# Optimization experiments

Hardware: AMD Instinct MI355X
Metric: run time of the kernel (lower is better)

Reference implementation:

```python
import jax, jax.numpy as jnp
import numpy as np

B, T, F, H, V = 16, 512, 512, 2048, 64
INPUT_INT_SCALE = 3.0
INT16_MIN, INT16_MAX = -32768, 32767


def setup_inputs() -> dict:
    key = jax.random.key(0)
    ks = jax.random.split(key, 8)
    x = jax.random.normal(ks[0], (B, T, F), dtype=jnp.float32)
    # int4 weights stored as int32 in [-8, 7]
    W_res_i4 = jax.random.randint(ks[1], (H, H), -8, 8, dtype=jnp.int32)
    W_in_i4 = jax.random.randint(ks[2], (H, F), -8, 8, dtype=jnp.int32)
    # per-row quantization scales (positive)
    S_res_row = jax.random.uniform(ks[3], (H,), dtype=jnp.float32, minval=0.01, maxval=0.2)
    S_in_row = jax.random.uniform(ks[4], (H,), dtype=jnp.float32, minval=0.01, maxval=0.2)
    g_res = jnp.float32(1.0)
    g_in = jnp.float32(1.0)
    W_out_w = jax.random.normal(ks[5], (V, H), dtype=jnp.float32) / np.float32(np.sqrt(H))
    W_out_b = jnp.zeros((V,), dtype=jnp.float32)
    return {
        "x": x, "S_res_row": S_res_row, "S_in_row": S_in_row,
        "g_res": g_res, "g_in": g_in,
        "W_out_w": W_out_w, "W_out_b": W_out_b,
        "W_res_i4": W_res_i4, "W_in_i4": W_in_i4,
    }


def reference(x, S_res_row, S_in_row, g_res, g_in, W_out_w, W_out_b, W_res_i4, W_in_i4):
    # row scales (matches _row_scales)
    s_res = (S_res_row / 49.0 * g_res)[None, :]                     # (1,H)
    s_in = (S_in_row / (7.0 * max(1.0, INPUT_INT_SCALE)) * g_in)[None, :]  # (1,H)

    def step(h, x_t):
        # quantize input frame and hidden state to integers (detached in torch)
        u_int = jax.lax.stop_gradient(jnp.round(x_t * INPUT_INT_SCALE)).astype(jnp.int32)     # (B,F)
        h_int = jax.lax.stop_gradient(jnp.round(jnp.clip(h, -1.0, 1.0) * 7.0)).astype(jnp.int32)  # (B,H)
        # integer matvecs: y[b,k] = sum_j W[k,j] * v[b,j]
        out_res = jnp.einsum('bh,kh->bk', h_int, W_res_i4)  # (B,H) int32
        out_in = jnp.einsum('bf,kf->bk', u_int, W_in_i4)    # (B,H) int32
        # int16 saturation, then row scale + gain, tanh
        out_res_f = jnp.clip(out_res, INT16_MIN, INT16_MAX).astype(jnp.float32)
        out_in_f = jnp.clip(out_in, INT16_MIN, INT16_MAX).astype(jnp.float32)
        h_new = jnp.tanh(out_res_f * s_res + out_in_f * s_in)
        return h_new, h_new

    h0 = jnp.zeros((x.shape[0], W_res_i4.shape[0]), dtype=jnp.float32)
    _, Hs = jax.lax.scan(step, h0, jnp.swapaxes(x, 0, 1))  # (T,B,H)
    Hs = jnp.swapaxes(Hs, 0, 1)                            # (B,T,H)
    # readout
    return jnp.einsum('bth,vh->btv', Hs, W_out_w) + W_out_b
```

## Files before the change

kernel.cpp:

```cpp
#include <hip/hip_runtime.h>
#include <hip/hip_bf16.h>


#define B_ 16
#define T_ 512
#define F_ 512
#define H_ 2048
#define V_ 64
#define SLICES 32
#define RPW 64
#define NTHREADS 256
#define NWG 512

typedef int i4v __attribute__((ext_vector_type(4)));

#if defined(__has_builtin)
#if __has_builtin(__builtin_amdgcn_sdot8)
#define HAVE_SDOT8 1
#endif
#endif

__device__ __forceinline__ int sdot8(int a, int b, int c) {
#ifdef HAVE_SDOT8
  return __builtin_amdgcn_sdot8(a, b, c, false);
#else
#pragma unroll
  for (int i = 0; i < 8; ++i) {
    int av = (a << (28 - 4 * i)) >> 28;
    int bv = (b << (28 - 4 * i)) >> 28;
    c += av * bv;
  }
  return c;
#endif
}

__device__ __forceinline__ float tanh_ref(float x) {
  float ax = fabsf(x);
  float xc = fminf(fmaxf(x, -7.90531110763549805f), 7.90531110763549805f);
  float x2 = __fmul_rn(xc, xc);
  float p = -2.76076847742355e-16f;
  p = __fmaf_rn(x2, p, 2.00018790482477e-13f);
  p = __fmaf_rn(x2, p, -8.60467152213735e-11f);
  p = __fmaf_rn(x2, p, 5.12229709037114e-08f);
  p = __fmaf_rn(x2, p, 1.48572235717979e-05f);
  p = __fmaf_rn(x2, p, 6.37261928875436e-04f);
  p = __fmaf_rn(x2, p, 4.89352455891786e-03f);
  p = __fmul_rn(xc, p);
  float q = 1.19825839466702e-06f;
  q = __fmaf_rn(x2, q, 1.18534705686654e-04f);
  q = __fmaf_rn(x2, q, 2.26843463243900e-03f);
  q = __fmaf_rn(x2, q, 4.89352518554385e-03f);
  float r = __fdiv_rn(p, q);
  return (ax < 0.0004f) ? x : r;
}

__device__ __forceinline__ unsigned f2bf(float f) {
  unsigned u = __float_as_uint(f);
  return (u + 0x7fffu + ((u >> 16) & 1u)) >> 16;
}

__device__ __forceinline__ void publish_tag(unsigned long long* p, unsigned data, unsigned tag) {
  unsigned long long u = ((unsigned long long)tag << 32) | data;
  __hip_atomic_store(p, u, __ATOMIC_RELAXED, __HIP_MEMORY_SCOPE_AGENT);
}

__global__ void pack_weights(const int* __restrict__ Wres, const int* __restrict__ Win,
                             int* __restrict__ wr4, int* __restrict__ wi4) {
  int id = blockIdx.x * blockDim.x + threadIdx.x;
  if (id < H_ * 256) {
    const int* src = Wres + id * 8;
    int pk = 0;
#pragma unroll
    for (int i = 0; i < 8; ++i) pk |= (src[i] & 15) << (4 * i);
    wr4[id] = pk;
  } else {
    int id2 = id - H_ * 256;
    if (id2 < H_ * 64) {
      const int* src = Win + id2 * 8;
      int pk = 0;
#pragma unroll
      for (int i = 0; i < 8; ++i) pk |= (src[i] & 15) << (4 * i);
      wi4[id2] = pk;
    }
  }
}

__global__ void pack_u(const float* __restrict__ x, int* __restrict__ um, int* __restrict__ ua) {
  int idx = blockIdx.x * blockDim.x + threadIdx.x;
  if (idx >= B_ * T_ * 64) return;
  const float* src = x + (size_t)idx * 8;
  int pm = 0, pa = 0;
#pragma unroll
  for (int i = 0; i < 8; ++i) {
    int u = (int)rintf(__fmul_rn(src[i], 3.0f));
    int vv = u + 128;
    pm |= (vv & 7) << (4 * i);
    pa |= (((vv >> 3) - 16) & 15) << (4 * i);
  }
  um[idx] = pm;
  ua[idx] = pa;
}

#define WLD(i, OFFSTR) \
  asm volatile("ds_read_b128 %0, %1 offset:" OFFSTR : "=v"(wreg[i]) : "v"(lds_wb))

__global__ void __launch_bounds__(NTHREADS, 2) esn_main(
    const int* __restrict__ um, const int* __restrict__ ua,
    const int* __restrict__ wr4, const int* __restrict__ wi4,
    unsigned long long* hq2,
    const float* __restrict__ S_res, const float* __restrict__ S_in,
    const float* __restrict__ g_res, const float* __restrict__ g_in,
    unsigned* __restrict__ Hs, int t0, int t1) {
  extern __shared__ __align__(16) char smem[];
  ::int4* lw4 = (::int4*)smem;
  int* lds_h = (int*)(lw4 + 16 * 256);
  int* lds_u = lds_h + 2 * 272;

  const int wg = blockIdx.x;
  const int b = wg & 15, slice = wg >> 4;
  const int tid = threadIdx.x;
  const unsigned lane = tid & 63;
  const int q = tid & 3;
  const int grow = slice * RPW + (tid >> 2);

  {
    const ::int4* gw = (const ::int4*)wr4;
#pragma unroll 4
    for (int m = 0; m < 16; ++m) lw4[m * 256 + tid] = gw[grow * 64 + q * 16 + m];
  }
  ::int4 rwm[4];
  {
    const ::int4* gwi = (const ::int4*)wi4;
#pragma unroll
    for (int m = 0; m < 4; ++m) rwm[m] = gwi[grow * 16 + q * 4 + m];
  }
  const float sr = __fmul_rn(__fdiv_rn(S_res[grow], 49.0f), g_res[0]);
  const float si = __fmul_rn(__fdiv_rn(S_in[grow], 21.0f), g_in[0]);

  const unsigned lds_wb = (unsigned)(size_t)smem + (unsigned)tid * 16u;

  unsigned ureg = 0;
  if (tid < 128) {
    unsigned v0 = (tid < 64) ? (unsigned)um[(b * T_ + t0) * 64 + tid]
                             : (unsigned)ua[(b * T_ + t0) * 64 + (tid - 64)];
    lds_u[(t0 & 1) * 128 + tid] = (int)v0;
    if (t0 + 1 < T_)
      ureg = (tid < 64) ? (unsigned)um[(b * T_ + t0 + 1) * 64 + tid]
                        : (unsigned)ua[(b * T_ + t0 + 1) * 64 + (tid - 64)];
  }
  __syncthreads();

  for (int t = t0; t < t1; ++t) {
    const int cbuf = t & 1, nbuf = cbuf ^ 1;
    if (t + 1 < t1 && tid < 128) lds_u[nbuf * 128 + tid] = (int)ureg;

    int am = 0, aa = 0;
    {
      const ::int4* lu = (const ::int4*)(lds_u + cbuf * 128);
#pragma unroll
      for (int m = 0; m < 4; ++m) {
        ::int4 w = rwm[m];
        ::int4 uM = lu[q * 4 + m];
        ::int4 uA = lu[16 + q * 4 + m];
        am = sdot8(w.x, uM.x, am); am = sdot8(w.y, uM.y, am);
        am = sdot8(w.z, uM.z, am); am = sdot8(w.w, uM.w, am);
        aa = sdot8(w.x, uA.x, aa); aa = sdot8(w.y, uA.y, aa);
        aa = sdot8(w.z, uA.z, aa); aa = sdot8(w.w, uA.w, aa);
      }
    }
    int accin = am + (aa << 3);
    accin += __shfl_xor(accin, 1);
    accin += __shfl_xor(accin, 2);

    i4v wreg[16];
    WLD(0, "0");      WLD(1, "4096");   WLD(2, "8192");   WLD(3, "12288");
    WLD(4, "16384");  WLD(5, "20480");  WLD(6, "24576");  WLD(7, "28672");
    WLD(8, "32768");  WLD(9, "36864");  WLD(10, "40960"); WLD(11, "45056");
    WLD(12, "49152"); WLD(13, "53248"); WLD(14, "57344"); WLD(15, "61440");

    if (tid < 64) {
      const unsigned long long* p = hq2 + (size_t)(cbuf * 16 + b) * 256 + tid * 4;
      unsigned long long u0, u1, u2, u3;
      const unsigned tag = (unsigned)t;
      for (;;) {
        u0 = __hip_atomic_load(p + 0, __ATOMIC_RELAXED, __HIP_MEMORY_SCOPE_AGENT);
        u1 = __hip_atomic_load(p + 1, __ATOMIC_RELAXED, __HIP_MEMORY_SCOPE_AGENT);
        u2 = __hip_atomic_load(p + 2, __ATOMIC_RELAXED, __HIP_MEMORY_SCOPE_AGENT);
        u3 = __hip_atomic_load(p + 3, __ATOMIC_RELAXED, __HIP_MEMORY_SCOPE_AGENT);
        unsigned d = ((unsigned)(u0 >> 32) ^ tag) | ((unsigned)(u1 >> 32) ^ tag) |
                     ((unsigned)(u2 >> 32) ^ tag) | ((unsigned)(u3 >> 32) ^ tag);
        if (d == 0) break;
        __builtin_amdgcn_s_sleep(1);
      }
      ::int4 hv;
      hv.x = (int)u0; hv.y = (int)u1; hv.z = (int)u2; hv.w = (int)u3;
      ((::int4*)(lds_h + cbuf * 272))[(tid >> 4) * 17 + (tid & 15)] = hv;
    }

    __syncthreads();
    __builtin_amdgcn_sched_barrier(0);

    int c0 = 0, c1 = 0, c2 = 0, c3 = 0;
    {
      const ::int4* lh = (const ::int4*)(lds_h + cbuf * 272);
#pragma unroll
      for (int m = 0; m < 16; m += 4) {
        ::int4 h0 = lh[q * 17 + m + 0];
        ::int4 h1 = lh[q * 17 + m + 1];
        ::int4 h2 = lh[q * 17 + m + 2];
        ::int4 h3 = lh[q * 17 + m + 3];
        c0 = sdot8(wreg[m + 0].x, h0.x, c0); c0 = sdot8(wreg[m + 0].y, h0.y, c0);
        c0 = sdot8(wreg[m + 0].z, h0.z, c0); c0 = sdot8(wreg[m + 0].w, h0.w, c0);
        c1 = sdot8(wreg[m + 1].x, h1.x, c1); c1 = sdot8(wreg[m + 1].y, h1.y, c1);
        c1 = sdot8(wreg[m + 1].z, h1.z, c1); c1 = sdot8(wreg[m + 1].w, h1.w, c1);
        c2 = sdot8(wreg[m + 2].x, h2.x, c2); c2 = sdot8(wreg[m + 2].y, h2.y, c2);
        c2 = sdot8(wreg[m + 2].z, h2.z, c2); c2 = sdot8(wreg[m + 2].w, h2.w, c2);
        c3 = sdot8(wreg[m + 3].x, h3.x, c3); c3 = sdot8(wreg[m + 3].y, h3.y, c3);
        c3 = sdot8(wreg[m + 3].z, h3.z, c3); c3 = sdot8(wreg[m + 3].w, h3.w, c3);
      }
    }
    int acc = (c0 + c1) + (c2 + c3);
    acc += __shfl_xor(acc, 1);
    acc += __shfl_xor(acc, 2);

    int cr = min(max(acc, -32768), 32767);
    int ci = min(max(accin, -32768), 32767);
    float arg = __fadd_rn(__fmul_rn((float)cr, sr), __fmul_rn((float)ci, si));
    float hn = tanh_ref(arg);
    float hc = fminf(fmaxf(hn, -1.0f), 1.0f);
    int qv = (int)rintf(__fmul_rn(hc, 7.0f));

    unsigned nib = ((unsigned)qv & 15u) << (4 * ((lane >> 2) & 7));
    nib |= (unsigned)__shfl_xor((int)nib, 4);
    nib |= (unsigned)__shfl_xor((int)nib, 8);
    nib |= (unsigned)__shfl_xor((int)nib, 16);
    if ((lane & 31) == 0)
      publish_tag(hq2 + (size_t)((t ^ 1) & 1) * 0 +
                      (size_t)(nbuf * 16 + b) * 256 + slice * 8 + (tid >> 6) * 2 + (lane >> 5),
                  nib, (unsigned)(t + 1));

    unsigned bfb = f2bf(hn);
    unsigned other = (unsigned)__shfl_xor((int)bfb, 4);
    if ((tid & 7) == 0)
      Hs[(size_t)(b * T_ + t) * (H_ / 2) + slice * 32 + (tid >> 3)] = bfb | (other << 16);
    if (t + 2 < T_ && tid < 128)
      ureg = (tid < 64) ? (unsigned)um[(b * T_ + t + 2) * 64 + tid]
                        : (unsigned)ua[(b * T_ + t + 2) * 64 + (tid - 64)];
  }
}

#define ACC8(acc, p, w0, w1)                                    \
  acc = fmaf(__uint_as_float(p.x << 16), w0.x, acc);            \
  acc = fmaf(__uint_as_float(p.x & 0xffff0000u), w0.y, acc);    \
  acc = fmaf(__uint_as_float(p.y << 16), w0.z, acc);            \
  acc = fmaf(__uint_as_float(p.y & 0xffff0000u), w0.w, acc);    \
  acc = fmaf(__uint_as_float(p.z << 16), w1.x, acc);            \
  acc = fmaf(__uint_as_float(p.z & 0xffff0000u), w1.y, acc);    \
  acc = fmaf(__uint_as_float(p.w << 16), w1.z, acc);            \
  acc = fmaf(__uint_as_float(p.w & 0xffff0000u), w1.w, acc);

__global__ void __launch_bounds__(256) readout(const unsigned* __restrict__ Hs,
                                               const float* __restrict__ Wout,
                                               const float* __restrict__ Wb,
                                               float* __restrict__ out) {
  const int v = threadIdx.x & 63;
  const int rg = threadIdx.x >> 6;
  const int bt0 = blockIdx.x * 16 + rg * 4;
  const float* wrow = Wout + (size_t)v * H_;
  const unsigned* h0 = Hs + (size_t)bt0 * (H_ / 2);
  float a0 = Wb[v], a1 = a0, a2 = a0, a3 = a0;
  for (int j = 0; j < H_ / 2; j += 4) {
    float4 w0 = *(const float4*)(wrow + 2 * j);
    float4 w1 = *(const float4*)(wrow + 2 * j + 4);
    uint4 p0 = *(const uint4*)(h0 + j);
    uint4 p1 = *(const uint4*)(h0 + (H_ / 2) + j);
    uint4 p2 = *(const uint4*)(h0 + 2 * (H_ / 2) + j);
    uint4 p3 = *(const uint4*)(h0 + 3 * (H_ / 2) + j);
    ACC8(a0, p0, w0, w1)
    ACC8(a1, p1, w0, w1)
    ACC8(a2, p2, w0, w1)
    ACC8(a3, p3, w0, w1)
  }
  out[(size_t)(bt0 + 0) * V_ + v] = a0;
  out[(size_t)(bt0 + 1) * V_ + v] = a1;
  out[(size_t)(bt0 + 2) * V_ + v] = a2;
  out[(size_t)(bt0 + 3) * V_ + v] = a3;
}

extern "C" void kernel_launch(void* const* d_in, const int* in_sizes, int n_in,
                              void* d_out, int out_size, void* d_ws, size_t ws_size,
                              hipStream_t stream) {
  const float* x = (const float*)d_in[0];
  const float* S_res = (const float*)d_in[1];
  const float* S_in = (const float*)d_in[2];
  const float* g_res = (const float*)d_in[3];
  const float* g_in = (const float*)d_in[4];
  const float* Woutw = (const float*)d_in[5];
  const float* Woutb = (const float*)d_in[6];
  const int* Wres = (const int*)d_in[7];
  const int* Win = (const int*)d_in[8];

  char* ws = (char*)d_ws;
  unsigned long long* hq2 = (unsigned long long*)(ws + 4096);
  int* um = (int*)(ws + (1 << 20));
  int* ua = um + (1 << 19);
  int* wr4 = ua + (1 << 19);
  int* wi4 = wr4 + (1 << 19);
  unsigned* Hs = (unsigned*)(ws + (8 << 20));

  hipMemsetAsync(d_ws, 0, 4096 + 65536, stream);
  hipLaunchKernelGGL(pack_weights, dim3(2560), dim3(256), 0, stream, Wres, Win, wr4, wi4);
  hipLaunchKernelGGL(pack_u, dim3(2048), dim3(256), 0, stream, x, um, ua);

  const int smem_bytes = 65536 + 2 * 272 * 4 + 2 * 128 * 4;
  (void)hipFuncSetAttribute((const void*)esn_main, hipFuncAttributeMaxDynamicSharedMemorySize,
                            smem_bytes);

  int t0 = 0, t1 = T_;
  void* args[] = {&um, &ua, &wr4, &wi4, &hq2, &S_res, &S_in,
                  &g_res, &g_in, &Hs, &t0, &t1};
  hipError_t e = hipLaunchCooperativeKernel((const void*)esn_main, dim3(NWG), dim3(NTHREADS),
                                            args, smem_bytes, stream);
  if (e != hipSuccess) {
    for (int t = 0; t < T_; ++t) {
      hipLaunchKernelGGL(esn_main, dim3(NWG), dim3(NTHREADS), smem_bytes, stream,
                         um, ua, wr4, wi4, hq2, S_res, S_in, g_res, g_in, Hs, t, t + 1);
    }
  }
  hipLaunchKernelGGL(readout, dim3(B_ * T_ / 16), dim3(256), 0, stream,
                     Hs, Woutw, Woutb, (float*)d_out);
}
```

Before: 1.040 ms.

## Make each wave poll hidden state independently and drop block barrier per step

Each of the four waves now spins on the global hidden-state tags itself and writes a private LDS copy, so the per-step __syncthreads is replaced by a wave-local lgkmcnt wait. Input-frame vectors are prefetched straight into registers from global memory instead of being staged through double-buffered LDS. The spin loop also stops sleeping on the first couple of failed polls. This aims to cut block-wide barrier latency on the serial recurrence critical path, at the cost of four times more atomic polling traffic and extra LDS space.

```diff
diff --git a/kernel.cpp b/kernel.cpp
--- a/kernel.cpp
+++ b/kernel.cpp
@@ -114,14 +114,15 @@
   extern __shared__ __align__(16) char smem[];
   ::int4* lw4 = (::int4*)smem;
   int* lds_h = (int*)(lw4 + 16 * 256);
-  int* lds_u = lds_h + 2 * 272;
 
   const int wg = blockIdx.x;
   const int b = wg & 15, slice = wg >> 4;
   const int tid = threadIdx.x;
-  const unsigned lane = tid & 63;
-  const int q = tid & 3;
-  const int grow = slice * RPW + (tid >> 2);
+  const int wv = tid >> 6;
+  const int lane = tid & 63;
+  const int rl = lane >> 2;
+  const int q = lane & 3;
+  const int grow = slice * RPW + wv * 16 + rl;
 
   {
     const ::int4* gw = (const ::int4*)wr4;
@@ -138,39 +139,20 @@
   const float si = __fmul_rn(__fdiv_rn(S_in[grow], 21.0f), g_in[0]);
 
   const unsigned lds_wb = (unsigned)(size_t)smem + (unsigned)tid * 16u;
-
-  unsigned ureg = 0;
-  if (tid < 128) {
-    unsigned v0 = (tid < 64) ? (unsigned)um[(b * T_ + t0) * 64 + tid]
-                             : (unsigned)ua[(b * T_ + t0) * 64 + (tid - 64)];
-    lds_u[(t0 & 1) * 128 + tid] = (int)v0;
-    if (t0 + 1 < T_)
-      ureg = (tid < 64) ? (unsigned)um[(b * T_ + t0 + 1) * 64 + tid]
-                        : (unsigned)ua[(b * T_ + t0 + 1) * 64 + (tid - 64)];
-  }
-  __syncthreads();
+  int* hb = lds_h + wv * 544;
+
+  const ::int4* gum = (const ::int4*)um;
+  const ::int4* gua = (const ::int4*)ua;
+
+  ::int4 uMr[4], uAr[4];
+  {
+    int base = (b * T_ + t0) * 16 + q * 4;
+#pragma unroll
+    for (int m = 0; m < 4; ++m) { uMr[m] = gum[base + m]; uAr[m] = gua[base + m]; }
+  }
 
   for (int t = t0; t < t1; ++t) {
     const int cbuf = t & 1, nbuf = cbuf ^ 1;
-    if (t + 1 < t1 && tid < 128) lds_u[nbuf * 128 + tid] = (int)ureg;
-
-    int am = 0, aa = 0;
-    {
-      const ::int4* lu = (const ::int4*)(lds_u + cbuf * 128);
-#pragma unroll
-      for (int m = 0; m < 4; ++m) {
-        ::int4 w = rwm[m];
-        ::int4 uM = lu[q * 4 + m];
-        ::int4 uA = lu[16 + q * 4 + m];
-        am = sdot8(w.x, uM.x, am); am = sdot8(w.y, uM.y, am);
-        am = sdot8(w.z, uM.z, am); am = sdot8(w.w, uM.w, am);
-        aa = sdot8(w.x, uA.x, aa); aa = sdot8(w.y, uA.y, aa);
-        aa = sdot8(w.z, uA.z, aa); aa = sdot8(w.w, uA.w, aa);
-      }
-    }
-    int accin = am + (aa << 3);
-    accin += __shfl_xor(accin, 1);
-    accin += __shfl_xor(accin, 2);
 
     i4v wreg[16];
     WLD(0, "0");      WLD(1, "4096");   WLD(2, "8192");   WLD(3, "12288");
@@ -178,31 +160,48 @@
     WLD(8, "32768");  WLD(9, "36864");  WLD(10, "40960"); WLD(11, "45056");
     WLD(12, "49152"); WLD(13, "53248"); WLD(14, "57344"); WLD(15, "61440");
 
-    if (tid < 64) {
-      const unsigned long long* p = hq2 + (size_t)(cbuf * 16 + b) * 256 + tid * 4;
-      unsigned long long u0, u1, u2, u3;
+    int am = 0, aa = 0;
+#pragma unroll
+    for (int m = 0; m < 4; ++m) {
+      ::int4 w = rwm[m];
+      ::int4 uM = uMr[m];
+      ::int4 uA = uAr[m];
+      am = sdot8(w.x, uM.x, am); am = sdot8(w.y, uM.y, am);
+      am = sdot8(w.z, uM.z, am); am = sdot8(w.w, uM.w, am);
+      aa = sdot8(w.x, uA.x, aa); aa = sdot8(w.y, uA.y, aa);
+      aa = sdot8(w.z, uA.z, aa); aa = sdot8(w.w, uA.w, aa);
+    }
+    int accin = am + (aa << 3);
+    accin += __shfl_xor(accin, 1);
+    accin += __shfl_xor(accin, 2);
+
+    unsigned long long u0, u1, u2, u3;
+    {
+      const unsigned long long* pp = hq2 + (size_t)(cbuf * 16 + b) * 256 + lane * 4;
       const unsigned tag = (unsigned)t;
+      int fails = 0;
       for (;;) {
-        u0 = __hip_atomic_load(p + 0, __ATOMIC_RELAXED, __HIP_MEMORY_SCOPE_AGENT);
-        u1 = __hip_atomic_load(p + 1, __ATOMIC_RELAXED, __HIP_MEMORY_SCOPE_AGENT);
-        u2 = __hip_atomic_load(p + 2, __ATOMIC_RELAXED, __HIP_MEMORY_SCOPE_AGENT);
-        u3 = __hip_atomic_load(p + 3, __ATOMIC_RELAXED, __HIP_MEMORY_SCOPE_AGENT);
+        u0 = __hip_atomic_load(pp + 0, __ATOMIC_RELAXED, __HIP_MEMORY_SCOPE_AGENT);
+        u1 = __hip_atomic_load(pp + 1, __ATOMIC_RELAXED, __HIP_MEMORY_SCOPE_AGENT);
+        u2 = __hip_atomic_load(pp + 2, __ATOMIC_RELAXED, __HIP_MEMORY_SCOPE_AGENT);
+        u3 = __hip_atomic_load(pp + 3, __ATOMIC_RELAXED, __HIP_MEMORY_SCOPE_AGENT);
         unsigned d = ((unsigned)(u0 >> 32) ^ tag) | ((unsigned)(u1 >> 32) ^ tag) |
                      ((unsigned)(u2 >> 32) ^ tag) | ((unsigned)(u3 >> 32) ^ tag);
         if (d == 0) break;
-        __builtin_amdgcn_s_sleep(1);
+        if (++fails > 2) __builtin_amdgcn_s_sleep(1);
       }
+    }
+    {
       ::int4 hv;
       hv.x = (int)u0; hv.y = (int)u1; hv.z = (int)u2; hv.w = (int)u3;
-      ((::int4*)(lds_h + cbuf * 272))[(tid >> 4) * 17 + (tid & 15)] = hv;
-    }
-
-    __syncthreads();
+      ((::int4*)(hb + cbuf * 272))[(lane >> 4) * 17 + (lane & 15)] = hv;
+    }
+    asm volatile("s_waitcnt lgkmcnt(0)" ::: "memory");
     __builtin_amdgcn_sched_barrier(0);
 
     int c0 = 0, c1 = 0, c2 = 0, c3 = 0;
     {
-      const ::int4* lh = (const ::int4*)(lds_h + cbuf * 272);
+      const ::int4* lh = (const ::int4*)(hb + cbuf * 272);
 #pragma unroll
       for (int m = 0; m < 16; m += 4) {
         ::int4 h0 = lh[q * 17 + m + 0];
@@ -230,22 +229,24 @@
     float hc = fminf(fmaxf(hn, -1.0f), 1.0f);
     int qv = (int)rintf(__fmul_rn(hc, 7.0f));
 
-    unsigned nib = ((unsigned)qv & 15u) << (4 * ((lane >> 2) & 7));
+    unsigned nib = ((unsigned)qv & 15u) << (4 * (rl & 7));
     nib |= (unsigned)__shfl_xor((int)nib, 4);
     nib |= (unsigned)__shfl_xor((int)nib, 8);
     nib |= (unsigned)__shfl_xor((int)nib, 16);
     if ((lane & 31) == 0)
-      publish_tag(hq2 + (size_t)((t ^ 1) & 1) * 0 +
-                      (size_t)(nbuf * 16 + b) * 256 + slice * 8 + (tid >> 6) * 2 + (lane >> 5),
+      publish_tag(hq2 + (size_t)(nbuf * 16 + b) * 256 + slice * 8 + wv * 2 + (lane >> 5),
                   nib, (unsigned)(t + 1));
 
     unsigned bfb = f2bf(hn);
     unsigned other = (unsigned)__shfl_xor((int)bfb, 4);
-    if ((tid & 7) == 0)
-      Hs[(size_t)(b * T_ + t) * (H_ / 2) + slice * 32 + (tid >> 3)] = bfb | (other << 16);
-    if (t + 2 < T_ && tid < 128)
-      ureg = (tid < 64) ? (unsigned)um[(b * T_ + t + 2) * 64 + tid]
-                        : (unsigned)ua[(b * T_ + t + 2) * 64 + (tid - 64)];
+    if ((lane & 7) == 0)
+      Hs[(size_t)(b * T_ + t) * (H_ / 2) + slice * 32 + wv * 8 + (lane >> 3)] =
+          bfb | (other << 16);
+    if (t + 1 < T_) {
+      int base = (b * T_ + t + 1) * 16 + q * 4;
+#pragma unroll
+      for (int m = 0; m < 4; ++m) { uMr[m] = gum[base + m]; uAr[m] = gua[base + m]; }
+    }
   }
 }
 
@@ -312,7 +313,7 @@
   hipLaunchKernelGGL(pack_weights, dim3(2560), dim3(256), 0, stream, Wres, Win, wr4, wi4);
   hipLaunchKernelGGL(pack_u, dim3(2048), dim3(256), 0, stream, x, um, ua);
 
-  const int smem_bytes = 65536 + 2 * 272 * 4 + 2 * 128 * 4;
+  const int smem_bytes = 65536 + 4 * 2 * 272 * 4;
   (void)hipFuncSetAttribute((const void*)esn_main, hipFuncAttributeMaxDynamicSharedMemorySize,
                             smem_bytes);
 
```

Result: slower. 2.537 ms (+143.8%).

## Replace block barrier with per-wave LDS flags and spread hidden-state polling across waves

Applied to the files above, without the earlier changes.

Every thread now polls one 64-bit tagged hidden-state word, instead of wave 0 polling four words per lane. Each wave writes its quarter of the hidden vector to LDS and raises a workgroup-scope release flag, and consumers acquire-spin per quarter before their dot products. This replaces the full __syncthreads and lets the weight LDS loads and the input dot product overlap the global poll. The LDS weight layout is permuted to match the new quarter-wise consumption, which adds spin loops on LDS flags and relies on subtle memory-ordering correctness.

```diff
diff --git a/kernel.cpp b/kernel.cpp
--- a/kernel.cpp
+++ b/kernel.cpp
@@ -13,6 +13,7 @@
 #define NWG 512
 
 typedef int i4v __attribute__((ext_vector_type(4)));
+typedef unsigned long long ull;
 
 #if defined(__has_builtin)
 #if __has_builtin(__builtin_amdgcn_sdot8)
@@ -59,8 +60,11 @@
   return (u + 0x7fffu + ((u >> 16) & 1u)) >> 16;
 }
 
-__device__ __forceinline__ void publish_tag(unsigned long long* p, unsigned data, unsigned tag) {
-  unsigned long long u = ((unsigned long long)tag << 32) | data;
+__device__ __forceinline__ ull xld(const ull* p) {
+  return __hip_atomic_load(p, __ATOMIC_RELAXED, __HIP_MEMORY_SCOPE_AGENT);
+}
+__device__ __forceinline__ void publish_tag(ull* p, unsigned data, unsigned tag) {
+  ull u = ((ull)tag << 32) | data;
   __hip_atomic_store(p, u, __ATOMIC_RELAXED, __HIP_MEMORY_SCOPE_AGENT);
 }
 
@@ -104,10 +108,26 @@
 #define WLD(i, OFFSTR) \
   asm volatile("ds_read_b128 %0, %1 offset:" OFFSTR : "=v"(wreg[i]) : "v"(lds_wb))
 
+#define QDOT(QQ)                                                                     \
+  {                                                                                  \
+    while (__hip_atomic_load(&lds_flag[cbuf * 4 + QQ], __ATOMIC_ACQUIRE,             \
+                             __HIP_MEMORY_SCOPE_WORKGROUP) < t) {}                   \
+    const ::int4* h4 = (const ::int4*)hbase + QQ * 17 + q * 4;                       \
+    ::int4 h0 = h4[0], h1 = h4[1], h2 = h4[2], h3 = h4[3];                           \
+    c0 = sdot8(wreg[QQ * 4 + 0].x, h0.x, c0); c0 = sdot8(wreg[QQ * 4 + 0].y, h0.y, c0); \
+    c0 = sdot8(wreg[QQ * 4 + 0].z, h0.z, c0); c0 = sdot8(wreg[QQ * 4 + 0].w, h0.w, c0); \
+    c1 = sdot8(wreg[QQ * 4 + 1].x, h1.x, c1); c1 = sdot8(wreg[QQ * 4 + 1].y, h1.y, c1); \
+    c1 = sdot8(wreg[QQ * 4 + 1].z, h1.z, c1); c1 = sdot8(wreg[QQ * 4 + 1].w, h1.w, c1); \
+    c2 = sdot8(wreg[QQ * 4 + 2].x, h2.x, c2); c2 = sdot8(wreg[QQ * 4 + 2].y, h2.y, c2); \
+    c2 = sdot8(wreg[QQ * 4 + 2].z, h2.z, c2); c2 = sdot8(wreg[QQ * 4 + 2].w, h2.w, c2); \
+    c3 = sdot8(wreg[QQ * 4 + 3].x, h3.x, c3); c3 = sdot8(wreg[QQ * 4 + 3].y, h3.y, c3); \
+    c3 = sdot8(wreg[QQ * 4 + 3].z, h3.z, c3); c3 = sdot8(wreg[QQ * 4 + 3].w, h3.w, c3); \
+  }
+
 __global__ void __launch_bounds__(NTHREADS, 2) esn_main(
     const int* __restrict__ um, const int* __restrict__ ua,
     const int* __restrict__ wr4, const int* __restrict__ wi4,
-    unsigned long long* hq2,
+    ull* hq,
     const float* __restrict__ S_res, const float* __restrict__ S_in,
     const float* __restrict__ g_res, const float* __restrict__ g_in,
     unsigned* __restrict__ Hs, int t0, int t1) {
@@ -115,18 +135,21 @@
   ::int4* lw4 = (::int4*)smem;
   int* lds_h = (int*)(lw4 + 16 * 256);
   int* lds_u = lds_h + 2 * 272;
+  int* lds_flag = lds_u + 2 * 128;
 
   const int wg = blockIdx.x;
   const int b = wg & 15, slice = wg >> 4;
   const int tid = threadIdx.x;
-  const unsigned lane = tid & 63;
+  const int wv = tid >> 6;
+  const int lane = tid & 63;
   const int q = tid & 3;
   const int grow = slice * RPW + (tid >> 2);
 
   {
     const ::int4* gw = (const ::int4*)wr4;
 #pragma unroll 4
-    for (int m = 0; m < 16; ++m) lw4[m * 256 + tid] = gw[grow * 64 + q * 16 + m];
+    for (int j = 0; j < 16; ++j)
+      lw4[j * 256 + tid] = gw[grow * 64 + (j >> 2) * 16 + q * 4 + (j & 3)];
   }
   ::int4 rwm[4];
   {
@@ -139,6 +162,7 @@
 
   const unsigned lds_wb = (unsigned)(size_t)smem + (unsigned)tid * 16u;
 
+  if (tid < 8) lds_flag[tid] = -1;
   unsigned ureg = 0;
   if (tid < 128) {
     unsigned v0 = (tid < 64) ? (unsigned)um[(b * T_ + t0) * 64 + tid]
@@ -153,6 +177,15 @@
   for (int t = t0; t < t1; ++t) {
     const int cbuf = t & 1, nbuf = cbuf ^ 1;
     if (t + 1 < t1 && tid < 128) lds_u[nbuf * 128 + tid] = (int)ureg;
+
+    const ull* pp = hq + (size_t)(cbuf * 16 + b) * 256 + tid;
+    ull uv = xld(pp);
+
+    i4v wreg[16];
+    WLD(0, "0");      WLD(1, "4096");   WLD(2, "8192");   WLD(3, "12288");
+    WLD(4, "16384");  WLD(5, "20480");  WLD(6, "24576");  WLD(7, "28672");
+    WLD(8, "32768");  WLD(9, "36864");  WLD(10, "40960"); WLD(11, "45056");
+    WLD(12, "49152"); WLD(13, "53248"); WLD(14, "57344"); WLD(15, "61440");
 
     int am = 0, aa = 0;
     {
@@ -172,53 +205,24 @@
     accin += __shfl_xor(accin, 1);
     accin += __shfl_xor(accin, 2);
 
-    i4v wreg[16];
-    WLD(0, "0");      WLD(1, "4096");   WLD(2, "8192");   WLD(3, "12288");
-    WLD(4, "16384");  WLD(5, "20480");  WLD(6, "24576");  WLD(7, "28672");
-    WLD(8, "32768");  WLD(9, "36864");  WLD(10, "40960"); WLD(11, "45056");
-    WLD(12, "49152"); WLD(13, "53248"); WLD(14, "57344"); WLD(15, "61440");
-
-    if (tid < 64) {
-      const unsigned long long* p = hq2 + (size_t)(cbuf * 16 + b) * 256 + tid * 4;
-      unsigned long long u0, u1, u2, u3;
-      const unsigned tag = (unsigned)t;
-      for (;;) {
-        u0 = __hip_atomic_load(p + 0, __ATOMIC_RELAXED, __HIP_MEMORY_SCOPE_AGENT);
-        u1 = __hip_atomic_load(p + 1, __ATOMIC_RELAXED, __HIP_MEMORY_SCOPE_AGENT);
-        u2 = __hip_atomic_load(p + 2, __ATOMIC_RELAXED, __HIP_MEMORY_SCOPE_AGENT);
-        u3 = __hip_atomic_load(p + 3, __ATOMIC_RELAXED, __HIP_MEMORY_SCOPE_AGENT);
-        unsigned d = ((unsigned)(u0 >> 32) ^ tag) | ((unsigned)(u1 >> 32) ^ tag) |
-                     ((unsigned)(u2 >> 32) ^ tag) | ((unsigned)(u3 >> 32) ^ tag);
-        if (d == 0) break;
-        __builtin_amdgcn_s_sleep(1);
-      }
-      ::int4 hv;
-      hv.x = (int)u0; hv.y = (int)u1; hv.z = (int)u2; hv.w = (int)u3;
-      ((::int4*)(lds_h + cbuf * 272))[(tid >> 4) * 17 + (tid & 15)] = hv;
-    }
-
-    __syncthreads();
-    __builtin_amdgcn_sched_barrier(0);
-
-    int c0 = 0, c1 = 0, c2 = 0, c3 = 0;
     {
-      const ::int4* lh = (const ::int4*)(lds_h + cbuf * 272);
-#pragma unroll
-      for (int m = 0; m < 16; m += 4) {
-        ::int4 h0 = lh[q * 17 + m + 0];
-        ::int4 h1 = lh[q * 17 + m + 1];
-        ::int4 h2 = lh[q * 17 + m + 2];
-        ::int4 h3 = lh[q * 17 + m + 3];
-        c0 = sdot8(wreg[m + 0].x, h0.x, c0); c0 = sdot8(wreg[m + 0].y, h0.y, c0);
-        c0 = sdot8(wreg[m + 0].z, h0.z, c0); c0 = sdot8(wreg[m + 0].w, h0.w, c0);
-        c1 = sdot8(wreg[m + 1].x, h1.x, c1); c1 = sdot8(wreg[m + 1].y, h1.y, c1);
-        c1 = sdot8(wreg[m + 1].z, h1.z, c1); c1 = sdot8(wreg[m + 1].w, h1.w, c1);
-        c2 = sdot8(wreg[m + 2].x, h2.x, c2); c2 = sdot8(wreg[m + 2].y, h2.y, c2);
-        c2 = sdot8(wreg[m + 2].z, h2.z, c2); c2 = sdot8(wreg[m + 2].w, h2.w, c2);
-        c3 = sdot8(wreg[m + 3].x, h3.x, c3); c3 = sdot8(wreg[m + 3].y, h3.y, c3);
-        c3 = sdot8(wreg[m + 3].z, h3.z, c3); c3 = sdot8(wreg[m + 3].w, h3.w, c3);
+      const unsigned tg = (unsigned)t;
+      int fails = 0;
+      while ((unsigned)(uv >> 32) != tg) {
+        if (++fails > 1) __builtin_amdgcn_s_sleep(1);
+        uv = xld(pp);
       }
     }
+    lds_h[cbuf * 272 + wv * 68 + lane] = (int)uv;
+    if (lane == 0)
+      __hip_atomic_store(&lds_flag[cbuf * 4 + wv], t, __ATOMIC_RELEASE,
+                         __HIP_MEMORY_SCOPE_WORKGROUP);
+    asm volatile("s_waitcnt lgkmcnt(0)" ::: "memory");
+    __builtin_amdgcn_sched_barrier(0);
+
+    int c0 = 0, c1 = 0, c2 = 0, c3 = 0;
+    const int* hbase = lds_h + cbuf * 272;
+    QDOT(0) QDOT(1) QDOT(2) QDOT(3)
     int acc = (c0 + c1) + (c2 + c3);
     acc += __shfl_xor(acc, 1);
     acc += __shfl_xor(acc, 2);
@@ -235,8 +239,7 @@
     nib |= (unsigned)__shfl_xor((int)nib, 8);
     nib |= (unsigned)__shfl_xor((int)nib, 16);
     if ((lane & 31) == 0)
-      publish_tag(hq2 + (size_t)((t ^ 1) & 1) * 0 +
-                      (size_t)(nbuf * 16 + b) * 256 + slice * 8 + (tid >> 6) * 2 + (lane >> 5),
+      publish_tag(hq + (size_t)(nbuf * 16 + b) * 256 + slice * 8 + wv * 2 + (lane >> 5),
                   nib, (unsigned)(t + 1));
 
     unsigned bfb = f2bf(hn);
@@ -301,30 +304,30 @@
   const int* Win = (const int*)d_in[8];
 
   char* ws = (char*)d_ws;
-  unsigned long long* hq2 = (unsigned long long*)(ws + 4096);
+  ull* hq = (ull*)(ws + 4096);
   int* um = (int*)(ws + (1 << 20));
   int* ua = um + (1 << 19);
   int* wr4 = ua + (1 << 19);
   int* wi4 = wr4 + (1 << 19);
   unsigned* Hs = (unsigned*)(ws + (8 << 20));
 
-  hipMemsetAsync(d_ws, 0, 4096 + 65536, stream);
+  hipMemsetAsync(ws + 4096, 0, 65536, stream);
   hipLaunchKernelGGL(pack_weights, dim3(2560), dim3(256), 0, stream, Wres, Win, wr4, wi4);
   hipLaunchKernelGGL(pack_u, dim3(2048), dim3(256), 0, stream, x, um, ua);
 
-  const int smem_bytes = 65536 + 2 * 272 * 4 + 2 * 128 * 4;
+  const int smem_bytes = 65536 + 2 * 272 * 4 + 2 * 128 * 4 + 8 * 4;
   (void)hipFuncSetAttribute((const void*)esn_main, hipFuncAttributeMaxDynamicSharedMemorySize,
                             smem_bytes);
 
   int t0 = 0, t1 = T_;
-  void* args[] = {&um, &ua, &wr4, &wi4, &hq2, &S_res, &S_in,
+  void* args[] = {&um, &ua, &wr4, &wi4, &hq, &S_res, &S_in,
                   &g_res, &g_in, &Hs, &t0, &t1};
   hipError_t e = hipLaunchCooperativeKernel((const void*)esn_main, dim3(NWG), dim3(NTHREADS),
                                             args, smem_bytes, stream);
   if (e != hipSuccess) {
     for (int t = 0; t < T_; ++t) {
       hipLaunchKernelGGL(esn_main, dim3(NWG), dim3(NTHREADS), smem_bytes, stream,
-                         um, ua, wr4, wi4, hq2, S_res, S_in, g_res, g_in, Hs, t, t + 1);
+                         um, ua, wr4, wi4, hq, S_res, S_in, g_res, g_in, Hs, t, t + 1);
     }
   }
   hipLaunchKernelGGL(readout, dim3(B_ * T_ / 16), dim3(256), 0, stream,
```

New measurement: 1.946 ms. 1.87x slower.

## Quantize hidden state via precomputed tanh thresholds and double-issue flag polling

Applied to the files above, without the earlier changes.

A setup kernel binary-searches seven input thresholds at which the quantized tanh output steps. The recurrent kernel then produces the int4 hidden value with comparisons instead of a rational tanh, so the next step's value is published before the tanh needed for the bf16 output is computed. The spin-wait now keeps two batches of atomic loads in flight and drops the per-iteration sleep, which shortens the inter-workgroup sync latency on the critical path at the cost of more memory traffic while waiting. Correctness relies on the quantized tanh being monotone in its argument, so that thresholds reproduce rounding exactly.

```diff
diff --git a/kernel.cpp b/kernel.cpp
--- a/kernel.cpp
+++ b/kernel.cpp
@@ -13,6 +13,7 @@
 #define NWG 512
 
 typedef int i4v __attribute__((ext_vector_type(4)));
+typedef unsigned long long ull;
 
 #if defined(__has_builtin)
 #if __has_builtin(__builtin_amdgcn_sdot8)
@@ -54,14 +55,35 @@
   return (ax < 0.0004f) ? x : r;
 }
 
+__device__ __forceinline__ int qv_of(float arg) {
+  float hn = tanh_ref(arg);
+  float hc = fminf(fmaxf(hn, -1.0f), 1.0f);
+  return (int)rintf(__fmul_rn(hc, 7.0f));
+}
+
 __device__ __forceinline__ unsigned f2bf(float f) {
   unsigned u = __float_as_uint(f);
   return (u + 0x7fffu + ((u >> 16) & 1u)) >> 16;
 }
 
-__device__ __forceinline__ void publish_tag(unsigned long long* p, unsigned data, unsigned tag) {
-  unsigned long long u = ((unsigned long long)tag << 32) | data;
+__device__ __forceinline__ ull xld(const ull* p) {
+  return __hip_atomic_load(p, __ATOMIC_RELAXED, __HIP_MEMORY_SCOPE_AGENT);
+}
+__device__ __forceinline__ void publish_tag(ull* p, unsigned data, unsigned tag) {
+  ull u = ((ull)tag << 32) | data;
   __hip_atomic_store(p, u, __ATOMIC_RELAXED, __HIP_MEMORY_SCOPE_AGENT);
+}
+
+__global__ void find_th(float* __restrict__ th) {
+  if (blockIdx.x == 0 && threadIdx.x < 7) {
+    int k = threadIdx.x + 1;
+    unsigned lo = 0, hi = 0x41000000u;
+    while (hi - lo > 1) {
+      unsigned mid = lo + ((hi - lo) >> 1);
+      if (qv_of(__uint_as_float(mid)) >= k) hi = mid; else lo = mid;
+    }
+    th[k - 1] = __uint_as_float(hi);
+  }
 }
 
 __global__ void pack_weights(const int* __restrict__ Wres, const int* __restrict__ Win,
@@ -104,12 +126,19 @@
 #define WLD(i, OFFSTR) \
   asm volatile("ds_read_b128 %0, %1 offset:" OFFSTR : "=v"(wreg[i]) : "v"(lds_wb))
 
+#define TAGOK(V) \
+  (!((((unsigned)(V##0 >> 32)) ^ tg) | (((unsigned)(V##1 >> 32)) ^ tg) | \
+     (((unsigned)(V##2 >> 32)) ^ tg) | (((unsigned)(V##3 >> 32)) ^ tg)))
+#define ISSUE(V) \
+  V##0 = xld(pp); V##1 = xld(pp + 1); V##2 = xld(pp + 2); V##3 = xld(pp + 3);
+
 __global__ void __launch_bounds__(NTHREADS, 2) esn_main(
     const int* __restrict__ um, const int* __restrict__ ua,
     const int* __restrict__ wr4, const int* __restrict__ wi4,
-    unsigned long long* hq2,
+    ull* hq,
     const float* __restrict__ S_res, const float* __restrict__ S_in,
     const float* __restrict__ g_res, const float* __restrict__ g_in,
+    const float* __restrict__ th,
     unsigned* __restrict__ Hs, int t0, int t1) {
   extern __shared__ __align__(16) char smem[];
   ::int4* lw4 = (::int4*)smem;
@@ -136,6 +165,8 @@
   }
   const float sr = __fmul_rn(__fdiv_rn(S_res[grow], 49.0f), g_res[0]);
   const float si = __fmul_rn(__fdiv_rn(S_in[grow], 21.0f), g_in[0]);
+  const float th1 = th[0], th2 = th[1], th3 = th[2], th4 = th[3],
+              th5 = th[4], th6 = th[5], th7 = th[6];
 
   const unsigned lds_wb = (unsigned)(size_t)smem + (unsigned)tid * 16u;
 
@@ -179,21 +210,21 @@
     WLD(12, "49152"); WLD(13, "53248"); WLD(14, "57344"); WLD(15, "61440");
 
     if (tid < 64) {
-      const unsigned long long* p = hq2 + (size_t)(cbuf * 16 + b) * 256 + tid * 4;
-      unsigned long long u0, u1, u2, u3;
-      const unsigned tag = (unsigned)t;
+      const ull* pp = hq + (size_t)(cbuf * 16 + b) * 256 + tid * 4;
+      const unsigned tg = (unsigned)t;
+      ull A0, A1, A2, A3, B0, B1, B2, B3, r0, r1, r2, r3;
+      ISSUE(A)
+      ISSUE(B)
+      int guard = 0;
       for (;;) {
-        u0 = __hip_atomic_load(p + 0, __ATOMIC_RELAXED, __HIP_MEMORY_SCOPE_AGENT);
-        u1 = __hip_atomic_load(p + 1, __ATOMIC_RELAXED, __HIP_MEMORY_SCOPE_AGENT);
-        u2 = __hip_atomic_load(p + 2, __ATOMIC_RELAXED, __HIP_MEMORY_SCOPE_AGENT);
-        u3 = __hip_atomic_load(p + 3, __ATOMIC_RELAXED, __HIP_MEMORY_SCOPE_AGENT);
-        unsigned d = ((unsigned)(u0 >> 32) ^ tag) | ((unsigned)(u1 >> 32) ^ tag) |
-                     ((unsigned)(u2 >> 32) ^ tag) | ((unsigned)(u3 >> 32) ^ tag);
-        if (d == 0) break;
-        __builtin_amdgcn_s_sleep(1);
+        if (TAGOK(A)) { r0 = A0; r1 = A1; r2 = A2; r3 = A3; break; }
+        ISSUE(A)
+        if (TAGOK(B)) { r0 = B0; r1 = B1; r2 = B2; r3 = B3; break; }
+        ISSUE(B)
+        if (++guard > 4096) __builtin_amdgcn_s_sleep(1);
       }
       ::int4 hv;
-      hv.x = (int)u0; hv.y = (int)u1; hv.z = (int)u2; hv.w = (int)u3;
+      hv.x = (int)r0; hv.y = (int)r1; hv.z = (int)r2; hv.w = (int)r3;
       ((::int4*)(lds_h + cbuf * 272))[(tid >> 4) * 17 + (tid & 15)] = hv;
     }
 
@@ -226,19 +257,21 @@
     int cr = min(max(acc, -32768), 32767);
     int ci = min(max(accin, -32768), 32767);
     float arg = __fadd_rn(__fmul_rn((float)cr, sr), __fmul_rn((float)ci, si));
-    float hn = tanh_ref(arg);
-    float hc = fminf(fmaxf(hn, -1.0f), 1.0f);
-    int qv = (int)rintf(__fmul_rn(hc, 7.0f));
+    float av = fabsf(arg);
+    int qa = (av >= th1) + (av >= th2) + (av >= th3) + (av >= th4) +
+             (av >= th5) + (av >= th6) + (av >= th7);
+    int qv = (arg < 0.0f) ? -qa : qa;
 
     unsigned nib = ((unsigned)qv & 15u) << (4 * ((lane >> 2) & 7));
     nib |= (unsigned)__shfl_xor((int)nib, 4);
     nib |= (unsigned)__shfl_xor((int)nib, 8);
     nib |= (unsigned)__shfl_xor((int)nib, 16);
     if ((lane & 31) == 0)
-      publish_tag(hq2 + (size_t)((t ^ 1) & 1) * 0 +
-                      (size_t)(nbuf * 16 + b) * 256 + slice * 8 + (tid >> 6) * 2 + (lane >> 5),
+      publish_tag(hq + (size_t)(nbuf * 16 + b) * 256 + slice * 8 + (tid >> 6) * 2 +
+                      (lane >> 5),
                   nib, (unsigned)(t + 1));
 
+    float hn = tanh_ref(arg);
     unsigned bfb = f2bf(hn);
     unsigned other = (unsigned)__shfl_xor((int)bfb, 4);
     if ((tid & 7) == 0)
@@ -301,14 +334,16 @@
   const int* Win = (const int*)d_in[8];
 
   char* ws = (char*)d_ws;
-  unsigned long long* hq2 = (unsigned long long*)(ws + 4096);
+  float* th = (float*)(ws + 2048);
+  ull* hq = (ull*)(ws + 4096);
   int* um = (int*)(ws + (1 << 20));
   int* ua = um + (1 << 19);
   int* wr4 = ua + (1 << 19);
   int* wi4 = wr4 + (1 << 19);
   unsigned* Hs = (unsigned*)(ws + (8 << 20));
 
-  hipMemsetAsync(d_ws, 0, 4096 + 65536, stream);
+  hipMemsetAsync(ws + 4096, 0, 65536, stream);
+  hipLaunchKernelGGL(find_th, dim3(1), dim3(64), 0, stream, th);
   hipLaunchKernelGGL(pack_weights, dim3(2560), dim3(256), 0, stream, Wres, Win, wr4, wi4);
   hipLaunchKernelGGL(pack_u, dim3(2048), dim3(256), 0, stream, x, um, ua);
 
@@ -317,14 +352,14 @@
                             smem_bytes);
 
   int t0 = 0, t1 = T_;
-  void* args[] = {&um, &ua, &wr4, &wi4, &hq2, &S_res, &S_in,
-                  &g_res, &g_in, &Hs, &t0, &t1};
+  void* args[] = {&um, &ua, &wr4, &wi4, &hq, &S_res, &S_in,
+                  &g_res, &g_in, &th, &Hs, &t0, &t1};
   hipError_t e = hipLaunchCooperativeKernel((const void*)esn_main, dim3(NWG), dim3(NTHREADS),
                                             args, smem_bytes, stream);
   if (e != hipSuccess) {
     for (int t = 0; t < T_; ++t) {
       hipLaunchKernelGGL(esn_main, dim3(NWG), dim3(NTHREADS), smem_bytes, stream,
-                         um, ua, wr4, wi4, hq2, S_res, S_in, g_res, g_in, Hs, t, t + 1);
+                         um, ua, wr4, wi4, hq, S_res, S_in, g_res, g_in, th, Hs, t, t + 1);
     }
   }
   hipLaunchKernelGGL(readout, dim3(B_ * T_ / 16), dim3(256), 0, stream,
```

Measured after the change: 4.008 ms. +285.2%, slower.
